# Optimization experiments

Measured on AMD Instinct MI355X. Metric: run time of the kernel, lower is better.

## Reference

```python
import jax, jax.numpy as jnp
import numpy as np

BETA = 1.0
CHANNELS = 1
RADIUS = 1


def _neighbour_sum(s, radius):
    # Plus-shaped stencil with circular boundary: sum of s shifted by
    # +-1..+-radius along H and along W (center excluded), matching the
    # circular-pad + cross-kernel conv2d in the torch module (channels=1).
    Js = jnp.zeros_like(s)
    for d in range(1, radius + 1):
        Js = Js + jnp.roll(s, d, axis=2) + jnp.roll(s, -d, axis=2)
        Js = Js + jnp.roll(s, d, axis=3) + jnp.roll(s, -d, axis=3)
    return Js


def setup_inputs() -> dict:
    key = jax.random.key(0)
    k1, k2, k3 = jax.random.split(key, 3)
    B, C, H, W = 16, CHANNELS, 2048, 2048
    x = jax.random.normal(k1, (B, C, H, W), dtype=jnp.float32)
    rand = jax.random.uniform(k2, (B, C, H, W), dtype=jnp.float32)
    drop_rand = jax.random.uniform(k3, (H, W), dtype=jnp.float32)
    return {"x": x, "rand": rand, "drop_rand": drop_rand}


def reference(x, rand, drop_rand):
    s = x[:, :CHANNELS]                       # [B,C,H,W]
    Js = _neighbour_sum(s, RADIUS)            # neighbour field
    delta_e = 2.0 * s * Js
    # flip probability: 1 if energy decreases, else Metropolis exp(-dE*beta)
    p = jnp.where(delta_e <= 0, jnp.ones_like(s), jnp.exp(-delta_e * BETA))
    dropout_mask = (drop_rand > 0.5)[None, None]  # [1,1,H,W] broadcast
    flip = -2.0 * jnp.logical_and(rand < p, dropout_mask).astype(s.dtype) + 1.0
    return s * flip
```

## Files before the change

kernel.cpp:

```cpp
#include <hip/hip_runtime.h>
#include <math.h>


namespace {

constexpr int Bn  = 16;
constexpr int Hn  = 2048;
constexpr int Wn  = 2048;
constexpr int W4  = Wn / 4;
constexpr int RPT = 4;
constexpr int HS  = Hn / RPT;
constexpr int NTHREADS = Bn * HS * W4;
constexpr int NBLK = NTHREADS / 256;
constexpr int NXCD = 8;
constexpr int BLK_PER_XCD = NBLK / NXCD;

typedef float f4 __attribute__((ext_vector_type(4)));

__global__ __launch_bounds__(256) void ising_flip_kernel(
    const float* __restrict__ x,
    const float* __restrict__ rnd,
    const float* __restrict__ drop,
    float* __restrict__ out)
{
    const int phys    = blockIdx.x;
    const int logical = (phys & (NXCD - 1)) * BLK_PER_XCD + (phys >> 3);
    const int tid     = logical * 256 + (int)threadIdx.x;
    const int lane    = (int)threadIdx.x & 63;

    const int wv = tid & (W4 - 1);
    const int hs = (tid >> 9) & (HS - 1);
    const int b  = tid >> 18;

    const int    c0  = wv * 4;
    const int    h0  = hs * RPT;
    const size_t img = (size_t)b * (size_t)(Hn * Wn);
    const float* xi  = x + img;

    f4 xr[RPT + 2];
#pragma unroll
    for (int k = 0; k < RPT + 2; ++k) {
        int hr = h0 - 1 + k;
        hr = (hr < 0) ? (Hn - 1) : ((hr >= Hn) ? 0 : hr);
        xr[k] = *(const f4*)(xi + (size_t)hr * Wn + c0);
    }

    f4 rv[RPT], dv[RPT];
#pragma unroll
    for (int i = 0; i < RPT; ++i) {
        const int row = (h0 + i) * Wn;
        rv[i] = __builtin_nontemporal_load((const f4*)(rnd + img + row + c0));
        dv[i] = *(const f4*)(drop + row + c0);
    }

    float lf[RPT], rt[RPT];
#pragma unroll
    for (int i = 0; i < RPT; ++i) {
        lf[i] = __shfl_up(xr[i + 1][3], 1);
        rt[i] = __shfl_down(xr[i + 1][0], 1);
    }
    if (lane == 0) {
        const int cl = (c0 == 0) ? (Wn - 1) : (c0 - 1);
#pragma unroll
        for (int i = 0; i < RPT; ++i) lf[i] = xi[(h0 + i) * Wn + cl];
    }
    if (lane == 63) {
        const int cr = (c0 + 4 == Wn) ? 0 : (c0 + 4);
#pragma unroll
        for (int i = 0; i < RPT; ++i) rt[i] = xi[(h0 + i) * Wn + cr];
    }

#pragma unroll
    for (int i = 0; i < RPT; ++i) {
        const f4 sc = xr[i + 1];
        const f4 up = xr[i];
        const f4 dn = xr[i + 2];
        f4 o;
#pragma unroll
        for (int j = 0; j < 4; ++j) {
            const float s     = sc[j];
            const float left  = (j == 0) ? lf[i] : sc[j - 1];
            const float right = (j == 3) ? rt[i] : sc[j + 1];
            const float js = ((up[j] + dn[j]) + left) + right;
            const float de = (2.0f * s) * js;

            bool lt;
            if (de <= 0.0f) {
                lt = true;
            } else {
                float p = expf(-de);
                if (fabsf(rv[i][j] - p) <= p * 1.0e-6f) {
                    p = (float)exp(-(double)de);
                }
                lt = rv[i][j] < p;
            }
            const bool flip = lt && (dv[i][j] > 0.5f);
            o[j] = flip ? -s : s;
        }
        __builtin_nontemporal_store(o, (f4*)(out + img + (size_t)(h0 + i) * Wn + c0));
    }
}

}

extern "C" void kernel_launch(void* const* d_in, const int* in_sizes, int n_in,
                              void* d_out, int out_size, void* d_ws, size_t ws_size,
                              hipStream_t stream)
{
    const float* x    = (const float*)d_in[0];
    const float* rnd  = (const float*)d_in[1];
    const float* drop = (const float*)d_in[2];
    float* out        = (float*)d_out;

    hipLaunchKernelGGL(ising_flip_kernel, dim3(NBLK), dim3(256), 0, stream,
                       x, rnd, drop, out);
}
```

Baseline: 151.4 us.

## Process 16-row strips per thread with register rolling and software prefetch

Each thread now walks a 16-row column strip in four 4-row steps, keeping halo rows in registers and carrying them from one step to the next. This cuts the redundant halo reads from 6/4 to about 18/16 per row. It also prefetches the next step's x and rand rows before computing the current one, so loads overlap compute. The cost is fewer blocks (4096) and higher register pressure, which may lower occupancy.

```diff
diff --git a/kernel.cpp b/kernel.cpp
--- a/kernel.cpp
+++ b/kernel.cpp
@@ -4,18 +4,46 @@
 
 namespace {
 
-constexpr int Bn  = 16;
-constexpr int Hn  = 2048;
-constexpr int Wn  = 2048;
-constexpr int W4  = Wn / 4;
-constexpr int RPT = 4;
-constexpr int HS  = Hn / RPT;
-constexpr int NTHREADS = Bn * HS * W4;
-constexpr int NBLK = NTHREADS / 256;
-constexpr int NXCD = 8;
-constexpr int BLK_PER_XCD = NBLK / NXCD;
+constexpr int Bn = 16;
+constexpr int Hn = 2048;
+constexpr int Wn = 2048;
+constexpr int IMG = Hn * Wn;
+constexpr int NBLK = 4096;
 
 typedef float f4 __attribute__((ext_vector_type(4)));
+
+__device__ __forceinline__ int wrapr(int r) {
+    return r < 0 ? r + Hn : (r >= Hn ? r - Hn : r);
+}
+
+__device__ __forceinline__ f4 flip_row(const f4 up, const f4 sc, const f4 dn,
+                                       const f4 rv, const f4 dv,
+                                       const float lf, const float rt)
+{
+    f4 o;
+#pragma unroll
+    for (int j = 0; j < 4; ++j) {
+        const float s     = sc[j];
+        const float left  = (j == 0) ? lf : sc[j - 1];
+        const float right = (j == 3) ? rt : sc[j + 1];
+        const float js = ((up[j] + dn[j]) + left) + right;
+        const float de = (2.0f * s) * js;
+
+        bool lt;
+        if (de <= 0.0f) {
+            lt = true;
+        } else {
+            float p = expf(-de);
+            if (fabsf(rv[j] - p) <= p * 1.0e-6f) {
+                p = (float)exp(-(double)de);
+            }
+            lt = rv[j] < p;
+        }
+        const bool flip = lt && (dv[j] > 0.5f);
+        o[j] = flip ? -s : s;
+    }
+    return o;
+}
 
 __global__ __launch_bounds__(256) void ising_flip_kernel(
     const float* __restrict__ x,
@@ -23,81 +51,79 @@
     const float* __restrict__ drop,
     float* __restrict__ out)
 {
-    const int phys    = blockIdx.x;
-    const int logical = (phys & (NXCD - 1)) * BLK_PER_XCD + (phys >> 3);
-    const int tid     = logical * 256 + (int)threadIdx.x;
-    const int lane    = (int)threadIdx.x & 63;
+    const int B    = blockIdx.x;
+    const int unit = (B & 7) * 512 + (B >> 3);
+    const int half = unit & 1;
+    const int gi   = unit >> 1;
+    const int b    = gi >> 7;
+    const int g    = gi & 127;
 
-    const int wv = tid & (W4 - 1);
-    const int hs = (tid >> 9) & (HS - 1);
-    const int b  = tid >> 18;
+    const int c0   = half * 1024 + (int)threadIdx.x * 4;
+    const int lane = (int)threadIdx.x & 63;
 
-    const int    c0  = wv * 4;
-    const int    h0  = hs * RPT;
-    const size_t img = (size_t)b * (size_t)(Hn * Wn);
+    const size_t img = (size_t)b * IMG;
     const float* xi  = x + img;
+    const int cl = (c0 == 0)      ? (Wn - 1) : (c0 - 1);
+    const int cr = (c0 + 4 == Wn) ? 0        : (c0 + 4);
 
-    f4 xr[RPT + 2];
+    int h0 = g * 16;
+
+    f4 r[6];
 #pragma unroll
-    for (int k = 0; k < RPT + 2; ++k) {
-        int hr = h0 - 1 + k;
-        hr = (hr < 0) ? (Hn - 1) : ((hr >= Hn) ? 0 : hr);
-        xr[k] = *(const f4*)(xi + (size_t)hr * Wn + c0);
-    }
-
-    f4 rv[RPT], dv[RPT];
+    for (int k = 0; k < 6; ++k)
+        r[k] = *(const f4*)(xi + (size_t)wrapr(h0 - 1 + k) * Wn + c0);
+    f4 rv[4];
 #pragma unroll
-    for (int i = 0; i < RPT; ++i) {
-        const int row = (h0 + i) * Wn;
-        rv[i] = __builtin_nontemporal_load((const f4*)(rnd + img + row + c0));
-        dv[i] = *(const f4*)(drop + row + c0);
-    }
-
-    float lf[RPT], rt[RPT];
-#pragma unroll
-    for (int i = 0; i < RPT; ++i) {
-        lf[i] = __shfl_up(xr[i + 1][3], 1);
-        rt[i] = __shfl_down(xr[i + 1][0], 1);
-    }
-    if (lane == 0) {
-        const int cl = (c0 == 0) ? (Wn - 1) : (c0 - 1);
-#pragma unroll
-        for (int i = 0; i < RPT; ++i) lf[i] = xi[(h0 + i) * Wn + cl];
-    }
-    if (lane == 63) {
-        const int cr = (c0 + 4 == Wn) ? 0 : (c0 + 4);
-#pragma unroll
-        for (int i = 0; i < RPT; ++i) rt[i] = xi[(h0 + i) * Wn + cr];
-    }
+    for (int i = 0; i < 4; ++i)
+        rv[i] = __builtin_nontemporal_load(
+            (const f4*)(rnd + img + (size_t)(h0 + i) * Wn + c0));
 
 #pragma unroll
-    for (int i = 0; i < RPT; ++i) {
-        const f4 sc = xr[i + 1];
-        const f4 up = xr[i];
-        const f4 dn = xr[i + 2];
-        f4 o;
+    for (int t = 0; t < 4; ++t) {
+        f4 nx[4], nrv[4];
+        if (t < 3) {
 #pragma unroll
-        for (int j = 0; j < 4; ++j) {
-            const float s     = sc[j];
-            const float left  = (j == 0) ? lf[i] : sc[j - 1];
-            const float right = (j == 3) ? rt[i] : sc[j + 1];
-            const float js = ((up[j] + dn[j]) + left) + right;
-            const float de = (2.0f * s) * js;
+            for (int k = 0; k < 4; ++k)
+                nx[k] = *(const f4*)(xi + (size_t)wrapr(h0 + 5 + k) * Wn + c0);
+#pragma unroll
+            for (int i = 0; i < 4; ++i)
+                nrv[i] = __builtin_nontemporal_load(
+                    (const f4*)(rnd + img + (size_t)(h0 + 4 + i) * Wn + c0));
+        }
 
-            bool lt;
-            if (de <= 0.0f) {
-                lt = true;
-            } else {
-                float p = expf(-de);
-                if (fabsf(rv[i][j] - p) <= p * 1.0e-6f) {
-                    p = (float)exp(-(double)de);
-                }
-                lt = rv[i][j] < p;
-            }
-            const bool flip = lt && (dv[i][j] > 0.5f);
-            o[j] = flip ? -s : s;
+        float lf[4], rt[4];
+#pragma unroll
+        for (int i = 0; i < 4; ++i) {
+            lf[i] = __shfl_up(r[i + 1][3], 1);
+            rt[i] = __shfl_down(r[i + 1][0], 1);
         }
-        __builtin_nontemporal_store(o, (f4*)(out + img + (size_t)(h0 + i) * Wn + c0));
+        if (lane == 0) {
+#pragma unroll
+            for (int i = 0; i < 4; ++i) lf[i] = xi[(size_t)(h0 + i) * Wn + cl];
+        }
+        if (lane == 63) {
+#pragma unroll
+            for (int i = 0; i < 4; ++i) rt[i] = xi[(size_t)(h0 + i) * Wn + cr];
+        }
+
+#pragma unroll
+        for (int i = 0; i < 4; ++i) {
+            const f4 dv = *(const f4*)(drop + (size_t)(h0 + i) * Wn + c0);
+            const f4 o  = flip_row(r[i], r[i + 1], r[i + 2], rv[i], dv,
+                                   lf[i], rt[i]);
+            __builtin_nontemporal_store(
+                o, (f4*)(out + img + (size_t)(h0 + i) * Wn + c0));
+        }
+
+        if (t < 3) {
+            r[0] = r[4];
+            r[1] = r[5];
+#pragma unroll
+            for (int k = 0; k < 4; ++k) r[2 + k] = nx[k];
+#pragma unroll
+            for (int i = 0; i < 4; ++i) rv[i] = nrv[i];
+            h0 += 4;
+        }
     }
 }
 
```

Measured after the change: 165.7 us. +9.4%, slower.
